# Performance work log

Measured on AMD Instinct MI355X. Metric: run time of the kernel, lower is better.

Reference implementation:

```python
import jax, jax.numpy as jnp
import numpy as np

ALPHA = 0.2      # LeakyReLU negative slope
NEG = -9e15     # mask fill value, as in pyGAT

B, N, NFEAT, NHID, NCLASS, NHEADS = 4, 2048, 128, 64, 32, 8


def setup_inputs() -> dict:
    key = jax.random.key(0)
    ks = jax.random.split(key, 8)
    x = jax.random.normal(ks[0], (B, N, NFEAT), dtype=jnp.float32)
    adj = jax.random.randint(ks[1], (B, N, N), 0, 2, dtype=jnp.int32)
    W = jax.random.normal(ks[2], (NHEADS, NFEAT, NHID), dtype=jnp.float32) * 0.1
    a1 = jax.random.normal(ks[3], (NHEADS, NHID), dtype=jnp.float32) * 0.1
    a2 = jax.random.normal(ks[4], (NHEADS, NHID), dtype=jnp.float32) * 0.1
    Wo = jax.random.normal(ks[5], (NHEADS * NHID, NCLASS), dtype=jnp.float32) * 0.1
    ao1 = jax.random.normal(ks[6], (NCLASS,), dtype=jnp.float32) * 0.1
    ao2 = jax.random.normal(ks[7], (NCLASS,), dtype=jnp.float32) * 0.1
    return {"x": x, "adj": adj, "W": W, "a1": a1, "a2": a2,
            "Wo": Wo, "ao1": ao1, "ao2": ao2}


def _gat_forward(x, adj, W, a1, a2, Wo, ao1, ao2):
    mask = adj > 0  # [B, N, N]
    # --- multi-head layer (concat=True) ---
    Wh = jnp.einsum('bnf,hfd->bhnd', x, W)          # [B,H,N,nhid]
    f1 = jnp.einsum('bhnd,hd->bhn', Wh, a1)          # Wh @ a[:nhid]
    f2 = jnp.einsum('bhnd,hd->bhn', Wh, a2)          # Wh @ a[nhid:]
    e = jax.nn.leaky_relu(f1[..., :, None] + f2[..., None, :], ALPHA)
    att = jax.nn.softmax(jnp.where(mask[:, None], e, NEG), axis=-1)
    h = jax.nn.elu(jnp.einsum('bhnm,bhmd->bhnd', att, Wh))  # [B,H,N,nhid]
    # torch.cat along dim=2: [B, N, H*nhid]
    h = jnp.transpose(h, (0, 2, 1, 3)).reshape(B, N, NHEADS * NHID)
    # (dropout layers are no-ops in eval mode)
    # --- output head (concat=False, no ELU) ---
    Wh2 = jnp.einsum('bnf,fc->bnc', h, Wo)           # [B,N,nclass]
    g1 = jnp.einsum('bnc,c->bn', Wh2, ao1)
    g2 = jnp.einsum('bnc,c->bn', Wh2, ao2)
    e2 = jax.nn.leaky_relu(g1[:, :, None] + g2[:, None, :], ALPHA)
    att2 = jax.nn.softmax(jnp.where(mask, e2, NEG), axis=-1)
    return jnp.einsum('bnm,bmc->bnc', att2, Wh2)     # [B,N,nclass]


def reference(x, adj, W, a1, a2, Wo, ao1, ao2):
    return _gat_forward(x, adj, W, a1, a2, Wo, ao1, ao2)
```

## Files before the change

kernel.cpp:

```cpp
#include <hip/hip_runtime.h>


typedef _Float16 half8  __attribute__((ext_vector_type(8)));
typedef _Float16 half2_ __attribute__((ext_vector_type(2)));
typedef float  float4_ __attribute__((ext_vector_type(4)));
typedef unsigned int uint4_ __attribute__((ext_vector_type(4)));

#if __has_builtin(__builtin_amdgcn_exp2f)
#define EXP2(x) __builtin_amdgcn_exp2f(x)
#else
#define EXP2(x) __expf((x) * 0.69314718055994531f)
#endif
#define LOG2E 1.44269504088896340f

static __device__ __forceinline__ unsigned pkh(float a, float b) {
#if __has_builtin(__builtin_amdgcn_cvt_pkrtz)
  return __builtin_bit_cast(unsigned, __builtin_amdgcn_cvt_pkrtz(a, b));
#else
  half2_ h = {(_Float16)a, (_Float16)b};
  return __builtin_bit_cast(unsigned, h);
#endif
}
static __device__ __forceinline__ unsigned short f2h(float f) {
  _Float16 h = (_Float16)f;
  return __builtin_bit_cast(unsigned short, h);
}

static __device__ __forceinline__ unsigned bitm(unsigned mb, int jj) {
#if __has_builtin(__builtin_amdgcn_sbfe)
  return (unsigned)__builtin_amdgcn_sbfe((int)mb, jj, 1);
#else
  return 0u - ((mb >> jj) & 1u);
#endif
}
static __device__ __forceinline__ unsigned pmask(unsigned s0, unsigned s1) {
  return __builtin_amdgcn_perm(s1, s0, 0x05040100u);
}
static __device__ __forceinline__ unsigned wmaxh(unsigned u, unsigned u2,
    unsigned pm, half2_ Ah, half2_ A2h) {
  half2_ p = Ah * __builtin_bit_cast(half2_, u);
  half2_ n = A2h * __builtin_bit_cast(half2_, u2);
  half2_ m = __builtin_elementwise_max(p, n);
  return __builtin_bit_cast(unsigned, m) & pm;
}

__global__ __launch_bounds__(256) void k_wfrag(
    const float* __restrict__ Wm, const float* __restrict__ Wo,
    unsigned short* __restrict__ Wf, unsigned short* __restrict__ WoF) {
  if (blockIdx.x < 32) {
    const int T = blockIdx.x * 256 + threadIdx.x;
    const int lane = T & 63;
    int r = T >> 6;
    const int nt = r & 3; r >>= 2;
    const int kstep = r & 3; r >>= 2;
    const int h = r;
    const int kk = kstep * 32 + (lane >> 4) * 8;
    const int n = nt * 16 + (lane & 15);
    const float* sp = Wm + h * 8192 + kk * 64 + n;
    unsigned short o[8];
    #pragma unroll
    for (int jj = 0; jj < 8; ++jj) o[jj] = f2h(sp[jj * 64]);
    *(uint4_*)(Wf + T * 8) = *(uint4_*)o;
  } else {
    const int T = (blockIdx.x - 32) * 256 + threadIdx.x;
    const int lane = T & 63;
    const int nt = (T >> 6) & 1, kstep = T >> 7;
    const int kk = kstep * 32 + (lane >> 4) * 8;
    const int n = nt * 16 + (lane & 15);
    unsigned short o[8];
    #pragma unroll
    for (int jj = 0; jj < 8; ++jj) o[jj] = f2h(Wo[(kk + jj) * 32 + n]);
    *(uint4_*)(WoF + T * 8) = *(uint4_*)o;
  }
}

__global__ __launch_bounds__(256) void k_front(
    const int* __restrict__ adj, unsigned long long* __restrict__ maskb,
    const float* __restrict__ x, const unsigned short* __restrict__ Wf,
    const float* __restrict__ a1, const float* __restrict__ a2,
    unsigned short* __restrict__ WhF, float* __restrict__ f1,
    unsigned short* __restrict__ Uv, unsigned short* __restrict__ U2v) {
  __shared__ float wsm[64 * 68];
  const int bx = blockIdx.x;
  const int t = threadIdx.x;
  if (bx >= 1024) {
    const int lane = t & 63, wid = t >> 6;
    const int s = lane & 15;
    const long long row0 = (long long)(bx - 1024) * 4;
    for (int rr = 0; rr < 4; ++rr) {
      const long long row = row0 + rr;
      const int4* src = (const int4*)(adj + row * 2048);
      #pragma unroll
      for (int c = 0; c < 2; ++c) {
        int4 v = src[c * 256 + t];
        unsigned nib = (v.x != 0 ? 1u : 0u) | (v.y != 0 ? 2u : 0u) |
                       (v.z != 0 ? 4u : 0u) | (v.w != 0 ? 8u : 0u);
        unsigned lo = (s < 8) ? (nib << (s * 4)) : 0u;
        unsigned hi = (s >= 8) ? (nib << ((s - 8) * 4)) : 0u;
        #pragma unroll
        for (int off = 1; off < 16; off <<= 1) {
          lo |= __shfl_xor(lo, off);
          hi |= __shfl_xor(hi, off);
        }
        if (s == 0) {
          int word = c * 16 + wid * 4 + (lane >> 4);
          maskb[row * 32 + word] = ((unsigned long long)hi << 32) | (unsigned long long)lo;
        }
      }
    }
    return;
  }
  const int itile = bx & 31, bh = bx >> 5;
  const int b = bh >> 3, h = bh & 7;
  const int i0 = itile * 64;
  const int lane = t & 63, w = t >> 6;
  const int cl = lane & 15, q = lane >> 4;
  const float* xrow = x + ((long long)b * 2048 + i0 + w * 16 + cl) * 128;
  const unsigned short* wfh = Wf + h * 8192;
  float4_ acc0 = {0.f, 0.f, 0.f, 0.f}, acc1 = acc0, acc2 = acc0, acc3 = acc0;
  #pragma unroll
  for (int kstep = 0; kstep < 4; ++kstep) {
    const float* xp = xrow + kstep * 32 + q * 8;
    const float4 xa = *(const float4*)xp;
    const float4 xb = *(const float4*)(xp + 4);
    uint4_ ap;
    ap.x = pkh(xa.x, xa.y);
    ap.y = pkh(xa.z, xa.w);
    ap.z = pkh(xb.x, xb.y);
    ap.w = pkh(xb.z, xb.w);
    const half8 af = __builtin_bit_cast(half8, ap);
    const unsigned short* bp = wfh + kstep * 2048 + lane * 8;
    const half8 b0 = *(const half8*)(bp);
    const half8 b1 = *(const half8*)(bp + 512);
    const half8 b2 = *(const half8*)(bp + 1024);
    const half8 b3 = *(const half8*)(bp + 1536);
    acc0 = __builtin_amdgcn_mfma_f32_16x16x32_f16(af, b0, acc0, 0, 0, 0);
    acc1 = __builtin_amdgcn_mfma_f32_16x16x32_f16(af, b1, acc1, 0, 0, 0);
    acc2 = __builtin_amdgcn_mfma_f32_16x16x32_f16(af, b2, acc2, 0, 0, 0);
    acc3 = __builtin_amdgcn_mfma_f32_16x16x32_f16(af, b3, acc3, 0, 0, 0);
  }
  {
    float4_ accs[4] = {acc0, acc1, acc2, acc3};
    #pragma unroll
    for (int nt = 0; nt < 4; ++nt)
      #pragma unroll
      for (int reg = 0; reg < 4; ++reg)
        wsm[(w * 16 + q * 4 + reg) * 68 + nt * 16 + cl] = accs[nt][reg];
  }
  __syncthreads();
  {
    const int row = t >> 2, seg = t & 3;
    const float* wr = wsm + row * 68 + seg * 16;
    const float4* a1p = (const float4*)(a1 + h * 64 + seg * 16);
    const float4* a2p = (const float4*)(a2 + h * 64 + seg * 16);
    float p1 = 0.f, p2 = 0.f;
    #pragma unroll
    for (int u = 0; u < 4; ++u) {
      const float4 wv = *(const float4*)(wr + u * 4);
      const float4 v1 = a1p[u];
      const float4 v2 = a2p[u];
      p1 += wv.x * v1.x + wv.y * v1.y + wv.z * v1.z + wv.w * v1.w;
      p2 += wv.x * v2.x + wv.y * v2.y + wv.z * v2.z + wv.w * v2.w;
    }
    p1 += __shfl_xor(p1, 1); p1 += __shfl_xor(p1, 2);
    p2 += __shfl_xor(p2, 1); p2 += __shfl_xor(p2, 2);
    if (seg == 0) {
      f1[(long long)bh * 2048 + i0 + row] = p1 * LOG2E;
      const float s2 = p2 * LOG2E;
      Uv[(long long)bh * 2048 + i0 + row] = f2h(EXP2(s2));
      U2v[(long long)bh * 2048 + i0 + row] = f2h(EXP2(0.2f * s2));
    }
  }
  #pragma unroll
  for (int u = 0; u < 2; ++u) {
    const int idx = u * 256 + t;
    const int l2 = idx & 63, nt2 = (idx >> 6) & 3, ks2 = idx >> 8;
    const int jrow = ks2 * 32 + (l2 >> 4) * 8;
    const int d = nt2 * 16 + (l2 & 15);
    uint4_ o;
    o.x = pkh(wsm[(jrow + 0) * 68 + d], wsm[(jrow + 1) * 68 + d]);
    o.y = pkh(wsm[(jrow + 2) * 68 + d], wsm[(jrow + 3) * 68 + d]);
    o.z = pkh(wsm[(jrow + 4) * 68 + d], wsm[(jrow + 5) * 68 + d]);
    o.w = pkh(wsm[(jrow + 6) * 68 + d], wsm[(jrow + 7) * 68 + d]);
    const long long off = (long long)bh * 131072 + (long long)itile * 4096 +
                          ks2 * 2048 + nt2 * 512 + l2 * 8;
    *(uint4_*)(WhF + off) = o;
  }
}

__global__ __launch_bounds__(256) void k_attn1(
    const unsigned short* __restrict__ whf, const float* __restrict__ f1v,
    const unsigned short* __restrict__ Uv, const unsigned short* __restrict__ U2v,
    const unsigned long long* __restrict__ maskb, unsigned short* __restrict__ hA) {
  __shared__ unsigned short bsm[2][8192];
  __shared__ unsigned short Us[2048], U2s[2048];
  const int bh = blockIdx.y, b = bh >> 3, hh = bh & 7;
  const int t = threadIdx.x;
  const int lane = t & 63, wid = t >> 6;
  const int cl = lane & 15, q = lane >> 4;
  const long long i_g = (long long)blockIdx.x * 64 + wid * 16 + cl;
  const float f1i = f1v[(long long)bh * 2048 + i_g];
  const float A = EXP2(f1i), A2 = EXP2(0.2f * f1i);
  const half2_ Ah = __builtin_bit_cast(half2_, pkh(A, A));
  const half2_ A2h = __builtin_bit_cast(half2_, pkh(A2, A2));
  const uint2* mpp = (const uint2*)(maskb + ((long long)b * 2048 + i_g) * 32);
  const unsigned short* whfb = whf + (long long)bh * 131072;
  const float4* gB = (const float4*)whfb;
  const half8 vones = {1.0f16, 1.0f16, 1.0f16, 1.0f16, 1.0f16, 1.0f16, 1.0f16, 1.0f16};
  ((uint4_*)Us)[t]  = ((const uint4_*)(Uv  + (long long)bh * 2048))[t];
  ((uint4_*)U2s)[t] = ((const uint4_*)(U2v + (long long)bh * 2048))[t];
  {
    float4 st0[4];
    #pragma unroll
    for (int u = 0; u < 4; ++u) st0[u] = gB[u * 256 + t];
    #pragma unroll
    for (int u = 0; u < 4; ++u) ((float4*)bsm[0])[u * 256 + t] = st0[u];
  }
  uint2 mw0_c = mpp[0], mw1_c = mpp[1];
  float4_ acc0 = {0.f, 0.f, 0.f, 0.f}, acc1 = acc0, acc2 = acc0, acc3 = acc0;
  float4_ accz = acc0;
  const int qs = q * 8;
  for (int s = 0; s < 16; ++s) {
    float4 stn0, stn1, stn2, stn3;
    if (s < 15) {
      const float4* gp = gB + (s + 1) * 1024 + t;
      stn0 = gp[0]; stn1 = gp[256]; stn2 = gp[512]; stn3 = gp[768];
    }
    const uint2 mwA = mw0_c, mwB = mw1_c;
    if (s < 15) { mw0_c = mpp[s * 2 + 2]; mw1_c = mpp[s * 2 + 3]; }
    __syncthreads();
    const unsigned short* bsb = bsm[s & 1] + lane * 8;
    #pragma unroll
    for (int jc2 = 0; jc2 < 2; ++jc2) {
      const int jc = s * 2 + jc2;
      const uint2 mw = jc2 ? mwB : mwA;
      #pragma unroll
      for (int ks = 0; ks < 2; ++ks) {
        const unsigned mb = (ks ? mw.y : mw.x) >> qs;
        const uint4_ uv  = *(const uint4_*)(Us  + jc * 64 + ks * 32 + qs);
        const uint4_ u2v = *(const uint4_*)(U2s + jc * 64 + ks * 32 + qs);
        const unsigned s0 = bitm(mb, 0), s1 = bitm(mb, 1), s2 = bitm(mb, 2),
                       s3 = bitm(mb, 3), s4 = bitm(mb, 4), s5 = bitm(mb, 5),
                       s6 = bitm(mb, 6), s7 = bitm(mb, 7);
        uint4_ pk;
        pk.x = wmaxh(uv.x, u2v.x, pmask(s0, s1), Ah, A2h);
        pk.y = wmaxh(uv.y, u2v.y, pmask(s2, s3), Ah, A2h);
        pk.z = wmaxh(uv.z, u2v.z, pmask(s4, s5), Ah, A2h);
        pk.w = wmaxh(uv.w, u2v.w, pmask(s6, s7), Ah, A2h);
        const half8 af = __builtin_bit_cast(half8, pk);
        const unsigned short* bp = bsb + (jc2 * 2 + ks) * 2048;
        const half8 b0 = *(const half8*)(bp);
        const half8 b1 = *(const half8*)(bp + 512);
        const half8 b2 = *(const half8*)(bp + 1024);
        const half8 b3 = *(const half8*)(bp + 1536);
        acc0 = __builtin_amdgcn_mfma_f32_16x16x32_f16(af, b0, acc0, 0, 0, 0);
        acc1 = __builtin_amdgcn_mfma_f32_16x16x32_f16(af, b1, acc1, 0, 0, 0);
        acc2 = __builtin_amdgcn_mfma_f32_16x16x32_f16(af, b2, acc2, 0, 0, 0);
        acc3 = __builtin_amdgcn_mfma_f32_16x16x32_f16(af, b3, acc3, 0, 0, 0);
        accz = __builtin_amdgcn_mfma_f32_16x16x32_f16(af, vones, accz, 0, 0, 0);
      }
    }
    if (s < 15) {
      float4* dp = (float4*)bsm[(s + 1) & 1] + t;
      dp[0] = stn0; dp[256] = stn1; dp[512] = stn2; dp[768] = stn3;
    }
  }
  __syncthreads();
  float* hs = (float*)bsm;
  {
    float4_ accs[4] = {acc0, acc1, acc2, acc3};
    #pragma unroll
    for (int reg = 0; reg < 4; ++reg) {
      const float rz = 1.f / accz[reg];
      #pragma unroll
      for (int nt = 0; nt < 4; ++nt) {
        float v = accs[nt][reg] * rz;
        v = (v > 0.f) ? v : (__expf(v) - 1.f);
        hs[(wid * 16 + q * 4 + reg) * 68 + nt * 16 + cl] = v;
      }
    }
  }
  __syncthreads();
  const int rtg0 = b * 128 + blockIdx.x * 4;
  #pragma unroll
  for (int u = 0; u < 2; ++u) {
    const int id = u * 256 + t;
    const int l2 = id & 63, ks2 = (id >> 6) & 1, rtile = id >> 7;
    const int rowl = rtile * 16 + (l2 & 15);
    const int d = ks2 * 32 + (l2 >> 4) * 8;
    const float* hp = hs + rowl * 68 + d;
    uint4_ o;
    o.x = pkh(hp[0], hp[1]); o.y = pkh(hp[2], hp[3]);
    o.z = pkh(hp[4], hp[5]); o.w = pkh(hp[6], hp[7]);
    const long long rt = rtg0 + rtile;
    const int kstep = hh * 2 + ks2;
    *(uint4_*)(hA + ((rt * 16 + kstep) * 64 + l2) * 8) = o;
  }
}

__global__ __launch_bounds__(128) void k_ogemm(
    const unsigned short* __restrict__ hA, const unsigned short* __restrict__ WoF,
    const float* __restrict__ ao1, const float* __restrict__ ao2,
    unsigned short* __restrict__ Wh2F, float* __restrict__ g1,
    unsigned short* __restrict__ gU, unsigned short* __restrict__ gU2) {
  __shared__ float w2s[32 * 36];
  const int t = threadIdx.x, lane = t & 63, wv = t >> 6;
  const int cl = lane & 15, q = lane >> 4;
  const long long rt = (long long)blockIdx.x * 2 + wv;
  float4_ acc0 = {0.f, 0.f, 0.f, 0.f}, acc1 = acc0;
  const unsigned short* ap = hA + rt * 8192 + lane * 8;
  const unsigned short* bp = WoF + lane * 8;
  #pragma unroll
  for (int kstep = 0; kstep < 16; ++kstep) {
    const half8 af = *(const half8*)(ap + kstep * 512);
    const half8 b0 = *(const half8*)(bp + kstep * 1024);
    const half8 b1 = *(const half8*)(bp + kstep * 1024 + 512);
    acc0 = __builtin_amdgcn_mfma_f32_16x16x32_f16(af, b0, acc0, 0, 0, 0);
    acc1 = __builtin_amdgcn_mfma_f32_16x16x32_f16(af, b1, acc1, 0, 0, 0);
  }
  const float o1a = ao1[cl], o1b = ao1[cl + 16];
  const float o2a = ao2[cl], o2b = ao2[cl + 16];
  #pragma unroll
  for (int reg = 0; reg < 4; ++reg) {
    const int rowl = wv * 16 + q * 4 + reg;
    w2s[rowl * 36 + cl] = acc0[reg];
    w2s[rowl * 36 + 16 + cl] = acc1[reg];
    float p1 = acc0[reg] * o1a + acc1[reg] * o1b;
    float p2 = acc0[reg] * o2a + acc1[reg] * o2b;
    p1 += __shfl_xor(p1, 1); p1 += __shfl_xor(p1, 2);
    p1 += __shfl_xor(p1, 4); p1 += __shfl_xor(p1, 8);
    p2 += __shfl_xor(p2, 1); p2 += __shfl_xor(p2, 2);
    p2 += __shfl_xor(p2, 4); p2 += __shfl_xor(p2, 8);
    if (cl == 0) {
      const long long row = (long long)blockIdx.x * 32 + rowl;
      g1[row] = p1 * LOG2E;
      const float s2 = p2 * LOG2E;
      gU[row]  = f2h(EXP2(s2));
      gU2[row] = f2h(EXP2(0.2f * s2));
    }
  }
  __syncthreads();
  {
    const int l2 = t & 63, nt2 = t >> 6;
    const int g = blockIdx.x >> 6, jc = (blockIdx.x >> 1) & 31, ks2 = blockIdx.x & 1;
    const int kb = (l2 >> 4) * 8, n = nt2 * 16 + (l2 & 15);
    uint4_ o;
    o.x = pkh(w2s[(kb + 0) * 36 + n], w2s[(kb + 1) * 36 + n]);
    o.y = pkh(w2s[(kb + 2) * 36 + n], w2s[(kb + 3) * 36 + n]);
    o.z = pkh(w2s[(kb + 4) * 36 + n], w2s[(kb + 5) * 36 + n]);
    o.w = pkh(w2s[(kb + 6) * 36 + n], w2s[(kb + 7) * 36 + n]);
    const long long off = (long long)g * 65536 + jc * 2048 + ks2 * 1024 +
                          nt2 * 512 + l2 * 8;
    *(uint4_*)(Wh2F + off) = o;
  }
}

__global__ __launch_bounds__(256) void k_attn2(
    const unsigned short* __restrict__ whf2, const float* __restrict__ g1v,
    const unsigned short* __restrict__ gU, const unsigned short* __restrict__ gU2,
    const unsigned long long* __restrict__ maskb, float* __restrict__ outp) {
  __shared__ float accs[4][16][33];
  __shared__ float zsh[64];
  const int b = blockIdx.y;
  const long long i0 = (long long)blockIdx.x * 16;
  const int t = threadIdx.x, lane = t & 63, wid = t >> 6;
  const int cl = lane & 15, q = lane >> 4;
  const float g1i = g1v[(long long)b * 2048 + i0 + cl];
  const float A = EXP2(g1i), A2 = EXP2(0.2f * g1i);
  const half2_ Ah = __builtin_bit_cast(half2_, pkh(A, A));
  const half2_ A2h = __builtin_bit_cast(half2_, pkh(A2, A2));
  const uint2* mpp = (const uint2*)(maskb + ((long long)b * 2048 + i0 + cl) * 32);
  const unsigned short* ub = gU + (long long)b * 2048;
  const unsigned short* u2b = gU2 + (long long)b * 2048;
  const unsigned short* wb = whf2 + (long long)b * 65536;
  const half8 vones = {1.0f16, 1.0f16, 1.0f16, 1.0f16, 1.0f16, 1.0f16, 1.0f16, 1.0f16};
  float4_ acc0 = {0.f, 0.f, 0.f, 0.f}, acc1 = acc0, accz = acc0;
  const int qs = q * 8;
  const int jc0 = wid * 8;
  uint2 mw_c = mpp[jc0];
  uint4_ ua_c  = *(const uint4_*)(ub  + jc0 * 64 + qs);
  uint4_ u2a_c = *(const uint4_*)(u2b + jc0 * 64 + qs);
  uint4_ ubn_c  = *(const uint4_*)(ub  + jc0 * 64 + 32 + qs);
  uint4_ u2b_c = *(const uint4_*)(u2b + jc0 * 64 + 32 + qs);
  for (int c8 = 0; c8 < 8; ++c8) {
    const int jc = jc0 + c8;
    const uint2 mw = mw_c;
    const uint4_ uA = ua_c, u2A = u2a_c, uB = ubn_c, u2B = u2b_c;
    {
      const int jn = jc + ((c8 < 7) ? 1 : 0);
      mw_c = mpp[jn];
      ua_c  = *(const uint4_*)(ub  + jn * 64 + qs);
      u2a_c = *(const uint4_*)(u2b + jn * 64 + qs);
      ubn_c  = *(const uint4_*)(ub  + jn * 64 + 32 + qs);
      u2b_c = *(const uint4_*)(u2b + jn * 64 + 32 + qs);
    }
    const unsigned short* bb = wb + (jc * 2) * 1024 + lane * 8;
    #pragma unroll
    for (int ks = 0; ks < 2; ++ks) {
      const unsigned mb = (ks ? mw.y : mw.x) >> qs;
      const uint4_ uv  = ks ? uB : uA;
      const uint4_ u2v = ks ? u2B : u2A;
      const unsigned s0 = bitm(mb, 0), s1 = bitm(mb, 1), s2 = bitm(mb, 2),
                     s3 = bitm(mb, 3), s4 = bitm(mb, 4), s5 = bitm(mb, 5),
                     s6 = bitm(mb, 6), s7 = bitm(mb, 7);
      uint4_ pk;
      pk.x = wmaxh(uv.x, u2v.x, pmask(s0, s1), Ah, A2h);
      pk.y = wmaxh(uv.y, u2v.y, pmask(s2, s3), Ah, A2h);
      pk.z = wmaxh(uv.z, u2v.z, pmask(s4, s5), Ah, A2h);
      pk.w = wmaxh(uv.w, u2v.w, pmask(s6, s7), Ah, A2h);
      const half8 af = __builtin_bit_cast(half8, pk);
      const unsigned short* bk = bb + ks * 1024;
      const half8 b0 = *(const half8*)bk;
      const half8 b1 = *(const half8*)(bk + 512);
      acc0 = __builtin_amdgcn_mfma_f32_16x16x32_f16(af, b0, acc0, 0, 0, 0);
      acc1 = __builtin_amdgcn_mfma_f32_16x16x32_f16(af, b1, acc1, 0, 0, 0);
      accz = __builtin_amdgcn_mfma_f32_16x16x32_f16(af, vones, accz, 0, 0, 0);
    }
  }
  if (cl == 0) {
    #pragma unroll
    for (int reg = 0; reg < 4; ++reg) zsh[wid * 16 + q * 4 + reg] = accz[reg];
  }
  float4_ a01[2] = {acc0, acc1};
  #pragma unroll
  for (int nt = 0; nt < 2; ++nt)
    #pragma unroll
    for (int reg = 0; reg < 4; ++reg)
      accs[wid][q * 4 + reg][nt * 16 + cl] = a01[nt][reg];
  __syncthreads();
  #pragma unroll
  for (int r = 0; r < 2; ++r) {
    int o = r * 256 + t;
    int il = o >> 5, c = o & 31;
    float s = accs[0][il][c] + accs[1][il][c] + accs[2][il][c] + accs[3][il][c];
    float Z = zsh[il] + zsh[16 + il] + zsh[32 + il] + zsh[48 + il];
    outp[((long long)b * 2048 + i0 + il) * 32 + c] = s / Z;
  }
}

extern "C" void kernel_launch(void* const* d_in, const int* in_sizes, int n_in,
                              void* d_out, int out_size, void* d_ws, size_t ws_size,
                              hipStream_t stream) {
  const float* x   = (const float*)d_in[0];
  const int*   adj = (const int*)d_in[1];
  const float* W   = (const float*)d_in[2];
  const float* a1  = (const float*)d_in[3];
  const float* a2  = (const float*)d_in[4];
  const float* Wo  = (const float*)d_in[5];
  const float* ao1 = (const float*)d_in[6];
  const float* ao2 = (const float*)d_in[7];
  float* out = (float*)d_out;
  char* ws = (char*)d_ws;

  unsigned long long* maskb = (unsigned long long*)(ws + 0);
  unsigned short* Wf   = (unsigned short*)(ws + 2097152);
  unsigned short* WoF  = (unsigned short*)(ws + 2228224);
  unsigned short* WhF  = (unsigned short*)(ws + 18874368);
  float* f1   = (float*)(ws + 27262976);
  unsigned short* Uv  = (unsigned short*)(ws + 27525120);
  unsigned short* U2v = (unsigned short*)(ws + 27656192);
  unsigned short* hA  = (unsigned short*)(ws + 27787264);
  unsigned short* Wh2F = (unsigned short*)(ws + 45613056);
  float* g1   = (float*)(ws + 46137344);
  unsigned short* gU  = (unsigned short*)(ws + 46170112);
  unsigned short* gU2 = (unsigned short*)(ws + 46186496);

  hipLaunchKernelGGL(k_wfrag, dim3(40), dim3(256), 0, stream, W, Wo, Wf, WoF);
  hipLaunchKernelGGL(k_front, dim3(3072), dim3(256), 0, stream, adj, maskb,
                     x, Wf, a1, a2, WhF, f1, Uv, U2v);
  hipLaunchKernelGGL(k_attn1, dim3(32, 32), dim3(256), 0, stream, WhF, f1, Uv, U2v,
                     maskb, hA);
  hipLaunchKernelGGL(k_ogemm, dim3(256), dim3(128), 0, stream, hA, WoF, ao1, ao2,
                     Wh2F, g1, gU, gU2);
  hipLaunchKernelGGL(k_attn2, dim3(128, 4), dim3(256), 0, stream, Wh2F, g1, gU, gU2,
                     maskb, out);
}
```

Measured before the change: 162.3 us.

## Give each attn1 wave two row tiles and stream U vectors per stage

k_attn1 now runs 128 threads per block, and each wave handles 32 rows as two 16-row MFMA tiles. Every B-fragment LDS read therefore feeds twice as many MFMAs, so there is half as much B traffic from LDS per unit of compute. The U/U2 vectors are staged into LDS alongside each B chunk rather than preloaded whole, and the sync moves to the end of each stage. The cost is more accumulator registers per thread and fewer waves per block to hide global-load latency.

New measurement: 166.7 us. 1.03x slower.

```diff
diff --git a/kernel.cpp b/kernel.cpp
--- a/kernel.cpp
+++ b/kernel.cpp
@@ -188,103 +188,143 @@
   }
 }
 
-__global__ __launch_bounds__(256) void k_attn1(
+__global__ __launch_bounds__(128) void k_attn1(
     const unsigned short* __restrict__ whf, const float* __restrict__ f1v,
     const unsigned short* __restrict__ Uv, const unsigned short* __restrict__ U2v,
     const unsigned long long* __restrict__ maskb, unsigned short* __restrict__ hA) {
-  __shared__ unsigned short bsm[2][8192];
-  __shared__ unsigned short Us[2048], U2s[2048];
+  __shared__ __align__(16) unsigned short bsm[2][8448];
   const int bh = blockIdx.y, b = bh >> 3, hh = bh & 7;
   const int t = threadIdx.x;
-  const int lane = t & 63, wid = t >> 6;
-  const int cl = lane & 15, q = lane >> 4;
-  const long long i_g = (long long)blockIdx.x * 64 + wid * 16 + cl;
-  const float f1i = f1v[(long long)bh * 2048 + i_g];
-  const float A = EXP2(f1i), A2 = EXP2(0.2f * f1i);
-  const half2_ Ah = __builtin_bit_cast(half2_, pkh(A, A));
-  const half2_ A2h = __builtin_bit_cast(half2_, pkh(A2, A2));
-  const uint2* mpp = (const uint2*)(maskb + ((long long)b * 2048 + i_g) * 32);
+  const int lane = t & 63, w = t >> 6;
+  const int cl = lane & 15, q = lane >> 4, qs = q * 8;
+  const long long rbase = (long long)bh * 2048;
+  const long long r0 = (long long)blockIdx.x * 64 + w * 32 + cl;
+  const float f10 = f1v[rbase + r0];
+  const float f11 = f1v[rbase + r0 + 16];
+  const float A0 = EXP2(f10), A20 = EXP2(0.2f * f10);
+  const float A1 = EXP2(f11), A21 = EXP2(0.2f * f11);
+  const half2_ Ah0  = __builtin_bit_cast(half2_, pkh(A0, A0));
+  const half2_ A2h0 = __builtin_bit_cast(half2_, pkh(A20, A20));
+  const half2_ Ah1  = __builtin_bit_cast(half2_, pkh(A1, A1));
+  const half2_ A2h1 = __builtin_bit_cast(half2_, pkh(A21, A21));
+  const uint2* mpp0 = (const uint2*)(maskb + ((long long)b * 2048 + r0) * 32);
+  const uint2* mpp1 = (const uint2*)(maskb + ((long long)b * 2048 + r0 + 16) * 32);
   const unsigned short* whfb = whf + (long long)bh * 131072;
   const float4* gB = (const float4*)whfb;
+  const unsigned* usrc = (const unsigned*)((t < 64 ? Uv : U2v) + rbase) + (t & 63);
   const half8 vones = {1.0f16, 1.0f16, 1.0f16, 1.0f16, 1.0f16, 1.0f16, 1.0f16, 1.0f16};
-  ((uint4_*)Us)[t]  = ((const uint4_*)(Uv  + (long long)bh * 2048))[t];
-  ((uint4_*)U2s)[t] = ((const uint4_*)(U2v + (long long)bh * 2048))[t];
   {
-    float4 st0[4];
-    #pragma unroll
-    for (int u = 0; u < 4; ++u) st0[u] = gB[u * 256 + t];
-    #pragma unroll
-    for (int u = 0; u < 4; ++u) ((float4*)bsm[0])[u * 256 + t] = st0[u];
-  }
-  uint2 mw0_c = mpp[0], mw1_c = mpp[1];
-  float4_ acc0 = {0.f, 0.f, 0.f, 0.f}, acc1 = acc0, acc2 = acc0, acc3 = acc0;
-  float4_ accz = acc0;
-  const int qs = q * 8;
+    const float4* gp = gB + t;
+    float4 s0 = gp[0], s1 = gp[128], s2 = gp[256], s3 = gp[384];
+    float4 s4 = gp[512], s5 = gp[640], s6 = gp[768], s7 = gp[896];
+    const unsigned u0 = usrc[0];
+    float4* dp = (float4*)bsm[0] + t;
+    dp[0] = s0; dp[128] = s1; dp[256] = s2; dp[384] = s3;
+    dp[512] = s4; dp[640] = s5; dp[768] = s6; dp[896] = s7;
+    ((unsigned*)bsm[0])[4096 + t] = u0;
+  }
+  uint2 m0a = mpp0[0], m0b = mpp0[1];
+  uint2 m1a = mpp1[0], m1b = mpp1[1];
+  float4_ a0_0 = {0.f, 0.f, 0.f, 0.f}, a0_1 = a0_0, a0_2 = a0_0, a0_3 = a0_0;
+  float4_ a1_0 = a0_0, a1_1 = a0_0, a1_2 = a0_0, a1_3 = a0_0;
+  float4_ az0 = a0_0, az1 = a0_0;
+  __syncthreads();
   for (int s = 0; s < 16; ++s) {
-    float4 stn0, stn1, stn2, stn3;
-    if (s < 15) {
-      const float4* gp = gB + (s + 1) * 1024 + t;
-      stn0 = gp[0]; stn1 = gp[256]; stn2 = gp[512]; stn3 = gp[768];
-    }
-    const uint2 mwA = mw0_c, mwB = mw1_c;
-    if (s < 15) { mw0_c = mpp[s * 2 + 2]; mw1_c = mpp[s * 2 + 3]; }
-    __syncthreads();
-    const unsigned short* bsb = bsm[s & 1] + lane * 8;
+    const int sn = (s < 15) ? (s + 1) : 15;
+    float4 st0, st1, st2, st3, st4, st5, st6, st7;
+    {
+      const float4* gp = gB + sn * 1024 + t;
+      st0 = gp[0]; st1 = gp[128]; st2 = gp[256]; st3 = gp[384];
+      st4 = gp[512]; st5 = gp[640]; st6 = gp[768]; st7 = gp[896];
+    }
+    const unsigned ustg = usrc[sn * 64];
+    const uint2 n0a = mpp0[sn * 2], n0b = mpp0[sn * 2 + 1];
+    const uint2 n1a = mpp1[sn * 2], n1b = mpp1[sn * 2 + 1];
+    const unsigned short* bs = bsm[s & 1];
+    const unsigned short* bsb = bs + lane * 8;
     #pragma unroll
     for (int jc2 = 0; jc2 < 2; ++jc2) {
-      const int jc = s * 2 + jc2;
-      const uint2 mw = jc2 ? mwB : mwA;
+      const uint2 mwf0 = jc2 ? m0b : m0a;
+      const uint2 mwf1 = jc2 ? m1b : m1a;
       #pragma unroll
       for (int ks = 0; ks < 2; ++ks) {
-        const unsigned mb = (ks ? mw.y : mw.x) >> qs;
-        const uint4_ uv  = *(const uint4_*)(Us  + jc * 64 + ks * 32 + qs);
-        const uint4_ u2v = *(const uint4_*)(U2s + jc * 64 + ks * 32 + qs);
-        const unsigned s0 = bitm(mb, 0), s1 = bitm(mb, 1), s2 = bitm(mb, 2),
-                       s3 = bitm(mb, 3), s4 = bitm(mb, 4), s5 = bitm(mb, 5),
-                       s6 = bitm(mb, 6), s7 = bitm(mb, 7);
-        uint4_ pk;
-        pk.x = wmaxh(uv.x, u2v.x, pmask(s0, s1), Ah, A2h);
-        pk.y = wmaxh(uv.y, u2v.y, pmask(s2, s3), Ah, A2h);
-        pk.z = wmaxh(uv.z, u2v.z, pmask(s4, s5), Ah, A2h);
-        pk.w = wmaxh(uv.w, u2v.w, pmask(s6, s7), Ah, A2h);
-        const half8 af = __builtin_bit_cast(half8, pk);
+        const int jin = jc2 * 64 + ks * 32 + qs;
+        const uint4_ uv  = *(const uint4_*)(bs + 8192 + jin);
+        const uint4_ u2v = *(const uint4_*)(bs + 8320 + jin);
         const unsigned short* bp = bsb + (jc2 * 2 + ks) * 2048;
         const half8 b0 = *(const half8*)(bp);
         const half8 b1 = *(const half8*)(bp + 512);
         const half8 b2 = *(const half8*)(bp + 1024);
         const half8 b3 = *(const half8*)(bp + 1536);
-        acc0 = __builtin_amdgcn_mfma_f32_16x16x32_f16(af, b0, acc0, 0, 0, 0);
-        acc1 = __builtin_amdgcn_mfma_f32_16x16x32_f16(af, b1, acc1, 0, 0, 0);
-        acc2 = __builtin_amdgcn_mfma_f32_16x16x32_f16(af, b2, acc2, 0, 0, 0);
-        acc3 = __builtin_amdgcn_mfma_f32_16x16x32_f16(af, b3, acc3, 0, 0, 0);
-        accz = __builtin_amdgcn_mfma_f32_16x16x32_f16(af, vones, accz, 0, 0, 0);
+        {
+          const unsigned mb = (ks ? mwf0.y : mwf0.x) >> qs;
+          const unsigned s0 = bitm(mb, 0), s1 = bitm(mb, 1), s2 = bitm(mb, 2),
+                         s3 = bitm(mb, 3), s4 = bitm(mb, 4), s5 = bitm(mb, 5),
+                         s6 = bitm(mb, 6), s7 = bitm(mb, 7);
+          uint4_ pk;
+          pk.x = wmaxh(uv.x, u2v.x, pmask(s0, s1), Ah0, A2h0);
+          pk.y = wmaxh(uv.y, u2v.y, pmask(s2, s3), Ah0, A2h0);
+          pk.z = wmaxh(uv.z, u2v.z, pmask(s4, s5), Ah0, A2h0);
+          pk.w = wmaxh(uv.w, u2v.w, pmask(s6, s7), Ah0, A2h0);
+          const half8 af = __builtin_bit_cast(half8, pk);
+          a0_0 = __builtin_amdgcn_mfma_f32_16x16x32_f16(af, b0, a0_0, 0, 0, 0);
+          a0_1 = __builtin_amdgcn_mfma_f32_16x16x32_f16(af, b1, a0_1, 0, 0, 0);
+          a0_2 = __builtin_amdgcn_mfma_f32_16x16x32_f16(af, b2, a0_2, 0, 0, 0);
+          a0_3 = __builtin_amdgcn_mfma_f32_16x16x32_f16(af, b3, a0_3, 0, 0, 0);
+          az0  = __builtin_amdgcn_mfma_f32_16x16x32_f16(af, vones, az0, 0, 0, 0);
+        }
+        {
+          const unsigned mb = (ks ? mwf1.y : mwf1.x) >> qs;
+          const unsigned s0 = bitm(mb, 0), s1 = bitm(mb, 1), s2 = bitm(mb, 2),
+                         s3 = bitm(mb, 3), s4 = bitm(mb, 4), s5 = bitm(mb, 5),
+                         s6 = bitm(mb, 6), s7 = bitm(mb, 7);
+          uint4_ pk;
+          pk.x = wmaxh(uv.x, u2v.x, pmask(s0, s1), Ah1, A2h1);
+          pk.y = wmaxh(uv.y, u2v.y, pmask(s2, s3), Ah1, A2h1);
+          pk.z = wmaxh(uv.z, u2v.z, pmask(s4, s5), Ah1, A2h1);
+          pk.w = wmaxh(uv.w, u2v.w, pmask(s6, s7), Ah1, A2h1);
+          const half8 af = __builtin_bit_cast(half8, pk);
+          a1_0 = __builtin_amdgcn_mfma_f32_16x16x32_f16(af, b0, a1_0, 0, 0, 0);
+          a1_1 = __builtin_amdgcn_mfma_f32_16x16x32_f16(af, b1, a1_1, 0, 0, 0);
+          a1_2 = __builtin_amdgcn_mfma_f32_16x16x32_f16(af, b2, a1_2, 0, 0, 0);
+          a1_3 = __builtin_amdgcn_mfma_f32_16x16x32_f16(af, b3, a1_3, 0, 0, 0);
+          az1  = __builtin_amdgcn_mfma_f32_16x16x32_f16(af, vones, az1, 0, 0, 0);
+        }
       }
     }
     if (s < 15) {
       float4* dp = (float4*)bsm[(s + 1) & 1] + t;
-      dp[0] = stn0; dp[256] = stn1; dp[512] = stn2; dp[768] = stn3;
-    }
-  }
-  __syncthreads();
+      dp[0] = st0; dp[128] = st1; dp[256] = st2; dp[384] = st3;
+      dp[512] = st4; dp[640] = st5; dp[768] = st6; dp[896] = st7;
+      ((unsigned*)bsm[(s + 1) & 1])[4096 + t] = ustg;
+    }
+    m0a = n0a; m0b = n0b; m1a = n1a; m1b = n1b;
+    __syncthreads();
+  }
   float* hs = (float*)bsm;
   {
-    float4_ accs[4] = {acc0, acc1, acc2, acc3};
+    float4_ acc0s[4] = {a0_0, a0_1, a0_2, a0_3};
+    float4_ acc1s[4] = {a1_0, a1_1, a1_2, a1_3};
     #pragma unroll
     for (int reg = 0; reg < 4; ++reg) {
-      const float rz = 1.f / accz[reg];
+      const float rz0 = 1.f / az0[reg];
+      const float rz1 = 1.f / az1[reg];
       #pragma unroll
       for (int nt = 0; nt < 4; ++nt) {
-        float v = accs[nt][reg] * rz;
-        v = (v > 0.f) ? v : (__expf(v) - 1.f);
-        hs[(wid * 16 + q * 4 + reg) * 68 + nt * 16 + cl] = v;
+        float v0 = acc0s[nt][reg] * rz0;
+        v0 = (v0 > 0.f) ? v0 : (__expf(v0) - 1.f);
+        hs[(w * 32 + q * 4 + reg) * 68 + nt * 16 + cl] = v0;
+        float v1 = acc1s[nt][reg] * rz1;
+        v1 = (v1 > 0.f) ? v1 : (__expf(v1) - 1.f);
+        hs[(w * 32 + 16 + q * 4 + reg) * 68 + nt * 16 + cl] = v1;
       }
     }
   }
   __syncthreads();
   const int rtg0 = b * 128 + blockIdx.x * 4;
   #pragma unroll
-  for (int u = 0; u < 2; ++u) {
-    const int id = u * 256 + t;
+  for (int u = 0; u < 4; ++u) {
+    const int id = u * 128 + t;
     const int l2 = id & 63, ks2 = (id >> 6) & 1, rtile = id >> 7;
     const int rowl = rtile * 16 + (l2 & 15);
     const int d = ks2 * 32 + (l2 >> 4) * 8;
@@ -468,7 +508,7 @@
   hipLaunchKernelGGL(k_wfrag, dim3(40), dim3(256), 0, stream, W, Wo, Wf, WoF);
   hipLaunchKernelGGL(k_front, dim3(3072), dim3(256), 0, stream, adj, maskb,
                      x, Wf, a1, a2, WhF, f1, Uv, U2v);
-  hipLaunchKernelGGL(k_attn1, dim3(32, 32), dim3(256), 0, stream, WhF, f1, Uv, U2v,
+  hipLaunchKernelGGL(k_attn1, dim3(32, 32), dim3(128), 0, stream, WhF, f1, Uv, U2v,
                      maskb, hA);
   hipLaunchKernelGGL(k_ogemm, dim3(256), dim3(128), 0, stream, hA, WoF, ao1, ao2,
                      Wh2F, g1, gU, gU2);
```

## Transpose bitmask layout and make attn1 waves process four row tiles each

Applied to the files above, without the earlier changes.

The packed adjacency bitmask is now stored column-word-major (word index outer, row inner), so lanes reading consecutive rows get coalesced loads. k_attn1 switches from 256-thread blocks that stage Wh fragments through double-buffered LDS with barriers to 128-thread blocks. Each wave now handles 64 rows (four 16-row fragments) and reads B fragments and U vectors straight from global memory, reusing each B load across four MFMA row tiles. This drops the LDS staging and per-step syncs and raises register use (16+4 accumulators). It also halves the grid to 512 blocks and relies on cache for the B operand.

After: 187.9 us. 15.8% more time.

```diff
diff --git a/kernel.cpp b/kernel.cpp
--- a/kernel.cpp
+++ b/kernel.cpp
@@ -103,8 +103,9 @@
           hi |= __shfl_xor(hi, off);
         }
         if (s == 0) {
-          int word = c * 16 + wid * 4 + (lane >> 4);
-          maskb[row * 32 + word] = ((unsigned long long)hi << 32) | (unsigned long long)lo;
+          const int word = c * 16 + wid * 4 + (lane >> 4);
+          maskb[(((row >> 11) * 32 + word) << 11) + (row & 2047)] =
+              ((unsigned long long)hi << 32) | (unsigned long long)lo;
         }
       }
     }
@@ -188,113 +189,106 @@
   }
 }
 
-__global__ __launch_bounds__(256) void k_attn1(
+__global__ __launch_bounds__(128) void k_attn1(
     const unsigned short* __restrict__ whf, const float* __restrict__ f1v,
     const unsigned short* __restrict__ Uv, const unsigned short* __restrict__ U2v,
     const unsigned long long* __restrict__ maskb, unsigned short* __restrict__ hA) {
-  __shared__ unsigned short bsm[2][8192];
-  __shared__ unsigned short Us[2048], U2s[2048];
+  __shared__ float hs[2][64 * 68];
   const int bh = blockIdx.y, b = bh >> 3, hh = bh & 7;
   const int t = threadIdx.x;
-  const int lane = t & 63, wid = t >> 6;
-  const int cl = lane & 15, q = lane >> 4;
-  const long long i_g = (long long)blockIdx.x * 64 + wid * 16 + cl;
-  const float f1i = f1v[(long long)bh * 2048 + i_g];
-  const float A = EXP2(f1i), A2 = EXP2(0.2f * f1i);
-  const half2_ Ah = __builtin_bit_cast(half2_, pkh(A, A));
-  const half2_ A2h = __builtin_bit_cast(half2_, pkh(A2, A2));
-  const uint2* mpp = (const uint2*)(maskb + ((long long)b * 2048 + i_g) * 32);
+  const int lane = t & 63, w = t >> 6;
+  const int cl = lane & 15, q = lane >> 4, qs = q * 8;
+  const int wbase = blockIdx.x * 128 + w * 64;
+  const long long rbase = (long long)bh * 2048;
+  const uint2* mT = (const uint2*)maskb;
+  const long long mbase = (long long)b * 32 * 2048;
+  int rowf[4];
+  half2_ Ah[4], A2h[4];
+  #pragma unroll
+  for (int f = 0; f < 4; ++f) {
+    const int rf = wbase + f * 16 + cl;
+    rowf[f] = rf;
+    const float f1i = f1v[rbase + rf];
+    const float A = EXP2(f1i), A2 = EXP2(0.2f * f1i);
+    Ah[f]  = __builtin_bit_cast(half2_, pkh(A, A));
+    A2h[f] = __builtin_bit_cast(half2_, pkh(A2, A2));
+  }
   const unsigned short* whfb = whf + (long long)bh * 131072;
-  const float4* gB = (const float4*)whfb;
+  const unsigned short* Ub  = Uv  + rbase;
+  const unsigned short* U2b = U2v + rbase;
   const half8 vones = {1.0f16, 1.0f16, 1.0f16, 1.0f16, 1.0f16, 1.0f16, 1.0f16, 1.0f16};
-  ((uint4_*)Us)[t]  = ((const uint4_*)(Uv  + (long long)bh * 2048))[t];
-  ((uint4_*)U2s)[t] = ((const uint4_*)(U2v + (long long)bh * 2048))[t];
-  {
-    float4 st0[4];
-    #pragma unroll
-    for (int u = 0; u < 4; ++u) st0[u] = gB[u * 256 + t];
-    #pragma unroll
-    for (int u = 0; u < 4; ++u) ((float4*)bsm[0])[u * 256 + t] = st0[u];
-  }
-  uint2 mw0_c = mpp[0], mw1_c = mpp[1];
-  float4_ acc0 = {0.f, 0.f, 0.f, 0.f}, acc1 = acc0, acc2 = acc0, acc3 = acc0;
-  float4_ accz = acc0;
-  const int qs = q * 8;
-  for (int s = 0; s < 16; ++s) {
-    float4 stn0, stn1, stn2, stn3;
-    if (s < 15) {
-      const float4* gp = gB + (s + 1) * 1024 + t;
-      stn0 = gp[0]; stn1 = gp[256]; stn2 = gp[512]; stn3 = gp[768];
-    }
-    const uint2 mwA = mw0_c, mwB = mw1_c;
-    if (s < 15) { mw0_c = mpp[s * 2 + 2]; mw1_c = mpp[s * 2 + 3]; }
-    __syncthreads();
-    const unsigned short* bsb = bsm[s & 1] + lane * 8;
-    #pragma unroll
-    for (int jc2 = 0; jc2 < 2; ++jc2) {
-      const int jc = s * 2 + jc2;
-      const uint2 mw = jc2 ? mwB : mwA;
+  float4_ acc[4][4];
+  float4_ az[4];
+  #pragma unroll
+  for (int f = 0; f < 4; ++f) {
+    az[f] = (float4_){0.f, 0.f, 0.f, 0.f};
+    #pragma unroll
+    for (int nt = 0; nt < 4; ++nt) acc[f][nt] = az[f];
+  }
+  #pragma unroll 2
+  for (int jc64 = 0; jc64 < 32; ++jc64) {
+    uint2 mF[4];
+    #pragma unroll
+    for (int f = 0; f < 4; ++f)
+      mF[f] = mT[mbase + (long long)jc64 * 2048 + rowf[f]];
+    #pragma unroll
+    for (int ks = 0; ks < 2; ++ks) {
+      const int jc32 = jc64 * 2 + ks;
+      const unsigned short* bp = whfb + jc32 * 2048 + lane * 8;
+      const half8 b0 = *(const half8*)(bp);
+      const half8 b1 = *(const half8*)(bp + 512);
+      const half8 b2 = *(const half8*)(bp + 1024);
+      const half8 b3 = *(const half8*)(bp + 1536);
+      const uint4_ uv  = *(const uint4_*)(Ub  + jc32 * 32 + qs);
+      const uint4_ u2v = *(const uint4_*)(U2b + jc32 * 32 + qs);
       #pragma unroll
-      for (int ks = 0; ks < 2; ++ks) {
-        const unsigned mb = (ks ? mw.y : mw.x) >> qs;
-        const uint4_ uv  = *(const uint4_*)(Us  + jc * 64 + ks * 32 + qs);
-        const uint4_ u2v = *(const uint4_*)(U2s + jc * 64 + ks * 32 + qs);
+      for (int f = 0; f < 4; ++f) {
+        const unsigned mb = (ks ? mF[f].y : mF[f].x) >> qs;
         const unsigned s0 = bitm(mb, 0), s1 = bitm(mb, 1), s2 = bitm(mb, 2),
                        s3 = bitm(mb, 3), s4 = bitm(mb, 4), s5 = bitm(mb, 5),
                        s6 = bitm(mb, 6), s7 = bitm(mb, 7);
         uint4_ pk;
-        pk.x = wmaxh(uv.x, u2v.x, pmask(s0, s1), Ah, A2h);
-        pk.y = wmaxh(uv.y, u2v.y, pmask(s2, s3), Ah, A2h);
-        pk.z = wmaxh(uv.z, u2v.z, pmask(s4, s5), Ah, A2h);
-        pk.w = wmaxh(uv.w, u2v.w, pmask(s6, s7), Ah, A2h);
+        pk.x = wmaxh(uv.x, u2v.x, pmask(s0, s1), Ah[f], A2h[f]);
+        pk.y = wmaxh(uv.y, u2v.y, pmask(s2, s3), Ah[f], A2h[f]);
+        pk.z = wmaxh(uv.z, u2v.z, pmask(s4, s5), Ah[f], A2h[f]);
+        pk.w = wmaxh(uv.w, u2v.w, pmask(s6, s7), Ah[f], A2h[f]);
         const half8 af = __builtin_bit_cast(half8, pk);
-        const unsigned short* bp = bsb + (jc2 * 2 + ks) * 2048;
-        const half8 b0 = *(const half8*)(bp);
-        const half8 b1 = *(const half8*)(bp + 512);
-        const half8 b2 = *(const half8*)(bp + 1024);
-        const half8 b3 = *(const half8*)(bp + 1536);
-        acc0 = __builtin_amdgcn_mfma_f32_16x16x32_f16(af, b0, acc0, 0, 0, 0);
-        acc1 = __builtin_amdgcn_mfma_f32_16x16x32_f16(af, b1, acc1, 0, 0, 0);
-        acc2 = __builtin_amdgcn_mfma_f32_16x16x32_f16(af, b2, acc2, 0, 0, 0);
-        acc3 = __builtin_amdgcn_mfma_f32_16x16x32_f16(af, b3, acc3, 0, 0, 0);
-        accz = __builtin_amdgcn_mfma_f32_16x16x32_f16(af, vones, accz, 0, 0, 0);
+        acc[f][0] = __builtin_amdgcn_mfma_f32_16x16x32_f16(af, b0, acc[f][0], 0, 0, 0);
+        acc[f][1] = __builtin_amdgcn_mfma_f32_16x16x32_f16(af, b1, acc[f][1], 0, 0, 0);
+        acc[f][2] = __builtin_amdgcn_mfma_f32_16x16x32_f16(af, b2, acc[f][2], 0, 0, 0);
+        acc[f][3] = __builtin_amdgcn_mfma_f32_16x16x32_f16(af, b3, acc[f][3], 0, 0, 0);
+        az[f]     = __builtin_amdgcn_mfma_f32_16x16x32_f16(af, vones, az[f], 0, 0, 0);
       }
     }
-    if (s < 15) {
-      float4* dp = (float4*)bsm[(s + 1) & 1] + t;
-      dp[0] = stn0; dp[256] = stn1; dp[512] = stn2; dp[768] = stn3;
-    }
-  }
-  __syncthreads();
-  float* hs = (float*)bsm;
-  {
-    float4_ accs[4] = {acc0, acc1, acc2, acc3};
+  }
+  float* hw = hs[w];
+  #pragma unroll
+  for (int f = 0; f < 4; ++f) {
     #pragma unroll
     for (int reg = 0; reg < 4; ++reg) {
-      const float rz = 1.f / accz[reg];
+      const float rz = 1.f / az[f][reg];
       #pragma unroll
       for (int nt = 0; nt < 4; ++nt) {
-        float v = accs[nt][reg] * rz;
+        float v = acc[f][nt][reg] * rz;
         v = (v > 0.f) ? v : (__expf(v) - 1.f);
-        hs[(wid * 16 + q * 4 + reg) * 68 + nt * 16 + cl] = v;
+        hw[(f * 16 + q * 4 + reg) * 68 + nt * 16 + cl] = v;
       }
     }
   }
   __syncthreads();
-  const int rtg0 = b * 128 + blockIdx.x * 4;
-  #pragma unroll
-  for (int u = 0; u < 2; ++u) {
-    const int id = u * 256 + t;
-    const int l2 = id & 63, ks2 = (id >> 6) & 1, rtile = id >> 7;
-    const int rowl = rtile * 16 + (l2 & 15);
-    const int d = ks2 * 32 + (l2 >> 4) * 8;
-    const float* hp = hs + rowl * 68 + d;
+  const int rtg0 = b * 128 + blockIdx.x * 8 + w * 4;
+  #pragma unroll
+  for (int u = 0; u < 8; ++u) {
+    const int ks2 = u & 1, rtile = u >> 1;
+    const int rowl = rtile * 16 + (lane & 15);
+    const int d = ks2 * 32 + (lane >> 4) * 8;
+    const float* hp = hw + rowl * 68 + d;
     uint4_ o;
     o.x = pkh(hp[0], hp[1]); o.y = pkh(hp[2], hp[3]);
     o.z = pkh(hp[4], hp[5]); o.w = pkh(hp[6], hp[7]);
     const long long rt = rtg0 + rtile;
     const int kstep = hh * 2 + ks2;
-    *(uint4_*)(hA + ((rt * 16 + kstep) * 64 + l2) * 8) = o;
+    *(uint4_*)(hA + ((rt * 16 + kstep) * 64 + lane) * 8) = o;
   }
 }
 
@@ -369,7 +363,9 @@
   const float A = EXP2(g1i), A2 = EXP2(0.2f * g1i);
   const half2_ Ah = __builtin_bit_cast(half2_, pkh(A, A));
   const half2_ A2h = __builtin_bit_cast(half2_, pkh(A2, A2));
-  const uint2* mpp = (const uint2*)(maskb + ((long long)b * 2048 + i0 + cl) * 32);
+  const uint2* mT = (const uint2*)maskb;
+  const int mrow = (int)(i0 + cl);
+  const long long mbase = (long long)b * 32 * 2048 + mrow;
   const unsigned short* ub = gU + (long long)b * 2048;
   const unsigned short* u2b = gU2 + (long long)b * 2048;
   const unsigned short* wb = whf2 + (long long)b * 65536;
@@ -377,7 +373,7 @@
   float4_ acc0 = {0.f, 0.f, 0.f, 0.f}, acc1 = acc0, accz = acc0;
   const int qs = q * 8;
   const int jc0 = wid * 8;
-  uint2 mw_c = mpp[jc0];
+  uint2 mw_c = mT[mbase + (long long)jc0 * 2048];
   uint4_ ua_c  = *(const uint4_*)(ub  + jc0 * 64 + qs);
   uint4_ u2a_c = *(const uint4_*)(u2b + jc0 * 64 + qs);
   uint4_ ubn_c  = *(const uint4_*)(ub  + jc0 * 64 + 32 + qs);
@@ -388,7 +384,7 @@
     const uint4_ uA = ua_c, u2A = u2a_c, uB = ubn_c, u2B = u2b_c;
     {
       const int jn = jc + ((c8 < 7) ? 1 : 0);
-      mw_c = mpp[jn];
+      mw_c = mT[mbase + (long long)jn * 2048];
       ua_c  = *(const uint4_*)(ub  + jn * 64 + qs);
       u2a_c = *(const uint4_*)(u2b + jn * 64 + qs);
       ubn_c  = *(const uint4_*)(ub  + jn * 64 + 32 + qs);
@@ -468,7 +464,7 @@
   hipLaunchKernelGGL(k_wfrag, dim3(40), dim3(256), 0, stream, W, Wo, Wf, WoF);
   hipLaunchKernelGGL(k_front, dim3(3072), dim3(256), 0, stream, adj, maskb,
                      x, Wf, a1, a2, WhF, f1, Uv, U2v);
-  hipLaunchKernelGGL(k_attn1, dim3(32, 32), dim3(256), 0, stream, WhF, f1, Uv, U2v,
+  hipLaunchKernelGGL(k_attn1, dim3(16, 32), dim3(128), 0, stream, WhF, f1, Uv, U2v,
                      maskb, hA);
   hipLaunchKernelGGL(k_ogemm, dim3(256), dim3(128), 0, stream, hA, WoF, ao1, ao2,
                      Wh2F, g1, gU, gU2);
```

## Transpose packed mask to column-major and read U vectors directly from global

Applied to the files above, without the earlier changes.

The packed adjacency bitmask is now stored word-major ([b][word][row]), so consecutive rows in a wave read consecutive 64-bit words and the mask loads in both attention kernels coalesce. The attention-1 kernel also stops staging the U/U2 vectors in shared memory and reads them from global/L1 inside the inner loop. The prefetch is made unconditional with the barrier moved to the top of the loop. These changes cut LDS use and uncoalesced mask traffic, at the cost of more global loads in the hot loop.

New measurement: 171.9 us. 5.9% more time.

```diff
diff --git a/kernel.cpp b/kernel.cpp
--- a/kernel.cpp
+++ b/kernel.cpp
@@ -103,8 +103,9 @@
           hi |= __shfl_xor(hi, off);
         }
         if (s == 0) {
-          int word = c * 16 + wid * 4 + (lane >> 4);
-          maskb[row * 32 + word] = ((unsigned long long)hi << 32) | (unsigned long long)lo;
+          const int word = c * 16 + wid * 4 + (lane >> 4);
+          maskb[(((row >> 11) * 32 + word) << 11) + (row & 2047)] =
+              ((unsigned long long)hi << 32) | (unsigned long long)lo;
         }
       }
     }
@@ -192,43 +193,39 @@
     const unsigned short* __restrict__ whf, const float* __restrict__ f1v,
     const unsigned short* __restrict__ Uv, const unsigned short* __restrict__ U2v,
     const unsigned long long* __restrict__ maskb, unsigned short* __restrict__ hA) {
-  __shared__ unsigned short bsm[2][8192];
-  __shared__ unsigned short Us[2048], U2s[2048];
+  __shared__ __align__(16) unsigned short bsm[2][8192];
   const int bh = blockIdx.y, b = bh >> 3, hh = bh & 7;
   const int t = threadIdx.x;
   const int lane = t & 63, wid = t >> 6;
-  const int cl = lane & 15, q = lane >> 4;
+  const int cl = lane & 15, q = lane >> 4, qs = q * 8;
   const long long i_g = (long long)blockIdx.x * 64 + wid * 16 + cl;
   const float f1i = f1v[(long long)bh * 2048 + i_g];
   const float A = EXP2(f1i), A2 = EXP2(0.2f * f1i);
   const half2_ Ah = __builtin_bit_cast(half2_, pkh(A, A));
   const half2_ A2h = __builtin_bit_cast(half2_, pkh(A2, A2));
-  const uint2* mpp = (const uint2*)(maskb + ((long long)b * 2048 + i_g) * 32);
+  const uint2* mT = (const uint2*)maskb;
+  const long long mbase = (long long)b * 65536 + i_g;
   const unsigned short* whfb = whf + (long long)bh * 131072;
+  const unsigned short* Ub  = Uv  + (long long)bh * 2048;
+  const unsigned short* U2b = U2v + (long long)bh * 2048;
   const float4* gB = (const float4*)whfb;
   const half8 vones = {1.0f16, 1.0f16, 1.0f16, 1.0f16, 1.0f16, 1.0f16, 1.0f16, 1.0f16};
-  ((uint4_*)Us)[t]  = ((const uint4_*)(Uv  + (long long)bh * 2048))[t];
-  ((uint4_*)U2s)[t] = ((const uint4_*)(U2v + (long long)bh * 2048))[t];
   {
-    float4 st0[4];
-    #pragma unroll
-    for (int u = 0; u < 4; ++u) st0[u] = gB[u * 256 + t];
-    #pragma unroll
-    for (int u = 0; u < 4; ++u) ((float4*)bsm[0])[u * 256 + t] = st0[u];
-  }
-  uint2 mw0_c = mpp[0], mw1_c = mpp[1];
+    const float4 s0 = gB[t], s1 = gB[256 + t], s2 = gB[512 + t], s3 = gB[768 + t];
+    float4* dp = (float4*)bsm[0] + t;
+    dp[0] = s0; dp[256] = s1; dp[512] = s2; dp[768] = s3;
+  }
+  uint2 mw0_c = mT[mbase], mw1_c = mT[mbase + 2048];
   float4_ acc0 = {0.f, 0.f, 0.f, 0.f}, acc1 = acc0, acc2 = acc0, acc3 = acc0;
   float4_ accz = acc0;
-  const int qs = q * 8;
   for (int s = 0; s < 16; ++s) {
-    float4 stn0, stn1, stn2, stn3;
-    if (s < 15) {
-      const float4* gp = gB + (s + 1) * 1024 + t;
-      stn0 = gp[0]; stn1 = gp[256]; stn2 = gp[512]; stn3 = gp[768];
-    }
+    __syncthreads();
+    const int sn = (s < 15) ? (s + 1) : 15;
+    const float4* gp = gB + sn * 1024 + t;
+    const float4 stn0 = gp[0], stn1 = gp[256], stn2 = gp[512], stn3 = gp[768];
     const uint2 mwA = mw0_c, mwB = mw1_c;
-    if (s < 15) { mw0_c = mpp[s * 2 + 2]; mw1_c = mpp[s * 2 + 3]; }
-    __syncthreads();
+    mw0_c = mT[mbase + (long long)(sn * 2) * 2048];
+    mw1_c = mT[mbase + (long long)(sn * 2 + 1) * 2048];
     const unsigned short* bsb = bsm[s & 1] + lane * 8;
     #pragma unroll
     for (int jc2 = 0; jc2 < 2; ++jc2) {
@@ -236,9 +233,9 @@
       const uint2 mw = jc2 ? mwB : mwA;
       #pragma unroll
       for (int ks = 0; ks < 2; ++ks) {
+        const uint4_ uv  = *(const uint4_*)(Ub  + jc * 64 + ks * 32 + qs);
+        const uint4_ u2v = *(const uint4_*)(U2b + jc * 64 + ks * 32 + qs);
         const unsigned mb = (ks ? mw.y : mw.x) >> qs;
-        const uint4_ uv  = *(const uint4_*)(Us  + jc * 64 + ks * 32 + qs);
-        const uint4_ u2v = *(const uint4_*)(U2s + jc * 64 + ks * 32 + qs);
         const unsigned s0 = bitm(mb, 0), s1 = bitm(mb, 1), s2 = bitm(mb, 2),
                        s3 = bitm(mb, 3), s4 = bitm(mb, 4), s5 = bitm(mb, 5),
                        s6 = bitm(mb, 6), s7 = bitm(mb, 7);
@@ -369,7 +366,9 @@
   const float A = EXP2(g1i), A2 = EXP2(0.2f * g1i);
   const half2_ Ah = __builtin_bit_cast(half2_, pkh(A, A));
   const half2_ A2h = __builtin_bit_cast(half2_, pkh(A2, A2));
-  const uint2* mpp = (const uint2*)(maskb + ((long long)b * 2048 + i0 + cl) * 32);
+  const uint2* mT = (const uint2*)maskb;
+  const int mrow = (int)(i0 + cl);
+  const long long mbase = (long long)b * 65536 + mrow;
   const unsigned short* ub = gU + (long long)b * 2048;
   const unsigned short* u2b = gU2 + (long long)b * 2048;
   const unsigned short* wb = whf2 + (long long)b * 65536;
@@ -377,7 +376,7 @@
   float4_ acc0 = {0.f, 0.f, 0.f, 0.f}, acc1 = acc0, accz = acc0;
   const int qs = q * 8;
   const int jc0 = wid * 8;
-  uint2 mw_c = mpp[jc0];
+  uint2 mw_c = mT[mbase + (long long)jc0 * 2048];
   uint4_ ua_c  = *(const uint4_*)(ub  + jc0 * 64 + qs);
   uint4_ u2a_c = *(const uint4_*)(u2b + jc0 * 64 + qs);
   uint4_ ubn_c  = *(const uint4_*)(ub  + jc0 * 64 + 32 + qs);
@@ -388,7 +387,7 @@
     const uint4_ uA = ua_c, u2A = u2a_c, uB = ubn_c, u2B = u2b_c;
     {
       const int jn = jc + ((c8 < 7) ? 1 : 0);
-      mw_c = mpp[jn];
+      mw_c = mT[mbase + (long long)jn * 2048];
       ua_c  = *(const uint4_*)(ub  + jn * 64 + qs);
       u2a_c = *(const uint4_*)(u2b + jn * 64 + qs);
       ubn_c  = *(const uint4_*)(ub  + jn * 64 + 32 + qs);
```
